# Performance work log

Hardware: AMD Instinct MI355X
Metric: run time of the kernel (lower is better)

The kernel has to match this reference:

```python
import jax, jax.numpy as jnp
import numpy as np

N = 65536      # total nodes (cells) in batch
E = 262144     # edges per edge type
T = 3          # edge types: row, col, diag
D = 128        # hidden_dim
HG = 4         # gat_heads
DHG = D // HG  # 32, GAT head dim
HH = 4         # hgt_heads
DHH = D // HH  # 32, HGT head dim
B = 32         # boards per batch
SLOPE = 0.2
EPS = 1e-6


def setup_inputs():
    ks = jax.random.split(jax.random.key(0), 32)
    def nrm(i, shape, s=0.05):
        return (jax.random.normal(ks[i], shape) * s).astype(jnp.float32)
    inp = {
        'x_cell': nrm(0, (N, D), 1.0),
        'z_h': nrm(1, (B, D), 1.0),
        'x_cell_embedded': nrm(2, (N, D), 1.0),
        'edge_index': jax.random.randint(ks[3], (T, 2, E), 0, N, dtype=jnp.int32),
        'batch_size': B,
        # GAT conv 1 (one GATConv per edge type, summed)
        'gat1_W': nrm(4, (T, D, D), 0.09),
        'gat1_asrc': nrm(5, (T, HG, DHG), 0.12),
        'gat1_adst': nrm(6, (T, HG, DHG), 0.12),
        'gat1_b': jnp.zeros((T, D), jnp.float32),
        # GAT conv 2
        'gat2_W': nrm(7, (T, D, D), 0.09),
        'gat2_asrc': nrm(8, (T, HG, DHG), 0.12),
        'gat2_adst': nrm(9, (T, HG, DHG), 0.12),
        'gat2_b': jnp.zeros((T, D), jnp.float32),
        # RMSNorms
        'norm1_s': jnp.ones((D,), jnp.float32),
        'norm2_s': jnp.ones((D,), jnp.float32),
        'norm3_s': jnp.ones((D,), jnp.float32),
        # HGT (single node type 'cell', T edge types)
        'hgt_Wk': nrm(10, (D, D), 0.09), 'hgt_bk': jnp.zeros((D,), jnp.float32),
        'hgt_Wq': nrm(11, (D, D), 0.09), 'hgt_bq': jnp.zeros((D,), jnp.float32),
        'hgt_Wv': nrm(12, (D, D), 0.09), 'hgt_bv': jnp.zeros((D,), jnp.float32),
        'hgt_arel': nrm(13, (T, HH, DHH, DHH), 0.15),
        'hgt_mrel': nrm(14, (T, HH, DHH, DHH), 0.15),
        'hgt_prel': jnp.ones((T, HH), jnp.float32),
        'hgt_Wo': nrm(15, (D, D), 0.09), 'hgt_bo': jnp.zeros((D,), jnp.float32),
        'hgt_skip': jnp.ones((), jnp.float32),
        # input injection
        'inj_W': nrm(16, (D, D), 0.09), 'inj_b': jnp.zeros((D,), jnp.float32),
        # FiLM
        'film_W1': nrm(17, (D, 2 * D), 0.09), 'film_b1': jnp.zeros((2 * D,), jnp.float32),
        'film_W2': nrm(18, (2 * D, 2 * D), 0.001), 'film_b2': jnp.zeros((2 * D,), jnp.float32),
    }
    return inp


def _rmsnorm(x, scale):
    return scale * x * jax.lax.rsqrt(jnp.mean(x * x, axis=-1, keepdims=True) + EPS)


def _res(x_old, x_new, scale):
    return jax.nn.leaky_relu(x_old + _rmsnorm(x_new, scale), SLOPE)


def _gat_sum(x, W, asrc, adst, b, src, dst):
    """HeteroConv(sum) over T GATConvs (concat heads, add_self_loops)."""
    loop = jnp.arange(N, dtype=src.dtype)
    def one(Wt, a_s, a_d, bt, s, t):
        s = jnp.concatenate([s, loop])   # self loops
        t = jnp.concatenate([t, loop])
        h = (x @ Wt).reshape(N, HG, DHG)             # [N,H,Dh]
        alpha_src = (h * a_s).sum(-1)                # [N,H]
        alpha_dst = (h * a_d).sum(-1)
        e = jax.nn.leaky_relu(alpha_src[s] + alpha_dst[t], SLOPE)  # [E+N,H]
        m = jax.ops.segment_max(e, t, num_segments=N)
        ex = jnp.exp(e - m[t])
        denom = jax.ops.segment_sum(ex, t, num_segments=N)
        alpha = ex / (denom[t] + 1e-16)
        out = jax.ops.segment_sum(alpha[:, :, None] * h[s], t, num_segments=N)
        return out.reshape(N, D) + bt
    return jax.vmap(one)(W, asrc, adst, b, src, dst).sum(0)


def _hgt(x, Wk, bk, Wq, bq, Wv, bv, a_rel, m_rel, p_rel, Wo, bo, skip, src, dst):
    k = (x @ Wk + bk).reshape(N, HH, DHH)
    q = (x @ Wq + bq).reshape(N, HH, DHH)
    v = (x @ Wv + bv).reshape(N, HH, DHH)
    # per-edge-type relation transforms at node level, then gather per edge
    k_t = jnp.einsum('nhd,thdf->tnhf', k, a_rel)    # [T,N,H,Dk]
    v_t = jnp.einsum('nhd,thdf->tnhf', v, m_rel)
    k_e = jax.vmap(lambda a, i: a[i])(k_t, src)     # [T,E,H,Dk]
    v_e = jax.vmap(lambda a, i: a[i])(v_t, src)
    score = (q[dst] * k_e).sum(-1) * p_rel[:, None, :] / np.sqrt(DHH)  # [T,E,H]
    score = score.reshape(T * E, HH)
    dst_f = dst.reshape(-1)
    m = jax.ops.segment_max(score, dst_f, num_segments=N)
    ex = jnp.exp(score - m[dst_f])
    denom = jax.ops.segment_sum(ex, dst_f, num_segments=N)
    alpha = ex / (denom[dst_f] + 1e-16)
    agg = jax.ops.segment_sum(alpha[:, :, None] * v_e.reshape(T * E, HH, DHH),
                              dst_f, num_segments=N)          # [N,H,Dk]
    out = jax.nn.gelu(agg.reshape(N, D), approximate=False) @ Wo + bo
    sig = jax.nn.sigmoid(skip)
    return sig * out + (1.0 - sig) * x


def _film(nodes, z_h, W1, b1, W2, b2, bsz):
    gb = jax.nn.gelu(z_h @ W1 + b1, approximate=False) @ W2 + b2  # [B,2D]
    gamma, beta = jnp.split(gb, 2, axis=-1)
    gamma = 0.1 * jnp.tanh(gamma)
    beta = 0.1 * jnp.tanh(beta)
    c = N // bsz
    out = (1.0 + gamma)[:, None, :] * nodes.reshape(bsz, c, D) + beta[:, None, :]
    return out.reshape(N, D)


def reference(x_cell, z_h, x_cell_embedded,
              gat1_W, gat1_asrc, gat1_adst, gat1_b,
              gat2_W, gat2_asrc, gat2_adst, gat2_b,
              norm1_s, norm2_s, norm3_s,
              hgt_Wk, hgt_bk, hgt_Wq, hgt_bq, hgt_Wv, hgt_bv,
              hgt_arel, hgt_mrel, hgt_prel, hgt_Wo, hgt_bo, hgt_skip,
              inj_W, inj_b, film_W1, film_b1, film_W2, film_b2,
              edge_index, batch_size):
    src = edge_index[:, 0]
    dst = edge_index[:, 1]
    x1 = _res(x_cell, _gat_sum(x_cell, gat1_W, gat1_asrc, gat1_adst, gat1_b, src, dst), norm1_s)
    x2 = _res(x1, _gat_sum(x1, gat2_W, gat2_asrc, gat2_adst, gat2_b, src, dst), norm2_s)
    x3 = _res(x2, _hgt(x2, hgt_Wk, hgt_bk, hgt_Wq, hgt_bq, hgt_Wv, hgt_bv,
                       hgt_arel, hgt_mrel, hgt_prel, hgt_Wo, hgt_bo, hgt_skip,
                       src, dst), norm3_s)
    x3 = x3 + x_cell_embedded @ inj_W + inj_b
    return _film(x3, z_h, film_W1, film_b1, film_W2, film_b2, batch_size)
```

## Files before the change

kernel.cpp:

```cpp
#include <hip/hip_runtime.h>

#define NN 65536
#define EE 262144
#define ND ((size_t)NN * 128)
#define TBW 132
#define WLP 136
#define NTOT (EE + NN)
#define CSRN (3*EE + 3*NN)

typedef unsigned short u16;
typedef short bf8_t __attribute__((ext_vector_type(8)));
typedef float f32x4 __attribute__((ext_vector_type(4)));

__device__ __forceinline__ float lrelu(float x){ return x > 0.f ? x : 0.2f*x; }
__device__ __forceinline__ float gelu_exact(float x){ return 0.5f*x*(1.f+erff(x*0.70710678118654752f)); }
__device__ __forceinline__ float fexp(float x){ return __expf(x); }
__device__ __forceinline__ u16 f2bf(float f){
    union { float f; unsigned u; } v; v.f = f;
    unsigned u = v.u;
    return (u16)((u + 0x7FFFu + ((u >> 16) & 1u)) >> 16);
}
__device__ __forceinline__ float bf2f(u16 b){
    union { unsigned u; float f; } v; v.u = ((unsigned)b) << 16; return v.f;
}
__device__ __forceinline__ float2 bf2x(unsigned p){
    union { unsigned u; float f; } a, b;
    a.u = (p & 0xFFFFu) << 16; b.u = p & 0xFFFF0000u;
    return make_float2(a.f, b.f);
}
__device__ __forceinline__ unsigned cvt2(float a, float b){
    unsigned r; asm("v_cvt_pk_bf16_f32 %0, %1, %2" : "=v"(r) : "v"(a), "v"(b)); return r;
}

__device__ __forceinline__ void load_af32(const float* __restrict__ X, int row, int lk, bf8_t* af){
    #pragma unroll
    for (int kk = 0; kk < 4; ++kk){
        const float* p = X + (size_t)row*128 + kk*32 + lk*8;
        float4 a = *(const float4*)p;
        float4 b = *(const float4*)(p+4);
        union { bf8_t v; unsigned u[4]; } r;
        r.u[0] = cvt2(a.x, a.y); r.u[1] = cvt2(a.z, a.w);
        r.u[2] = cvt2(b.x, b.y); r.u[3] = cvt2(b.z, b.w);
        af[kk] = r.v;
    }
}
__device__ __forceinline__ void load_af16(const u16* __restrict__ X, int row, int lk, bf8_t* af){
    #pragma unroll
    for (int kk = 0; kk < 4; ++kk)
        af[kk] = *(const bf8_t*)(X + (size_t)row*128 + kk*32 + lk*8);
}

__device__ __forceinline__ void stage_w(const u16* __restrict__ src, u16* __restrict__ wl, int tid){
    #pragma unroll
    for (int j = 0; j < 8; ++j){
        int o = (j*256 + tid)*8;
        bf8_t v = *(const bf8_t*)(src + o);
        *(bf8_t*)(wl + ((o>>7)*WLP + (o&127))) = v;
    }
}

__device__ __forceinline__ void mfma_l1_acc(const bf8_t* af, const u16* __restrict__ wl,
                                            int lr, int lk, f32x4* acc){
    #pragma unroll
    for (int kk = 0; kk < 4; ++kk){
        bf8_t B[8];
        #pragma unroll
        for (int nt = 0; nt < 8; ++nt)
            B[nt] = *(const bf8_t*)&wl[(nt*16+lr)*WLP + kk*32 + lk*8];
        #pragma unroll
        for (int nt = 0; nt < 8; ++nt)
            acc[nt] = __builtin_amdgcn_mfma_f32_16x16x32_bf16(af[kk], B[nt], acc[nt], 0, 0, 0);
    }
}
__device__ __forceinline__ void mfma_l1(const bf8_t* af, const u16* __restrict__ wl,
                                        int lr, int lk, f32x4* acc){
    #pragma unroll
    for (int i = 0; i < 8; ++i) acc[i] = (f32x4){0.f,0.f,0.f,0.f};
    mfma_l1_acc(af, wl, lr, lk, acc);
}
__device__ __forceinline__ void mfma_l2(const bf8_t* af0, const bf8_t* af1,
                                        const u16* __restrict__ wl,
                                        int lr, int lk, f32x4* acc0, f32x4* acc1){
    #pragma unroll
    for (int i = 0; i < 8; ++i){ acc0[i] = (f32x4){0.f,0.f,0.f,0.f}; acc1[i] = (f32x4){0.f,0.f,0.f,0.f}; }
    #pragma unroll
    for (int kk = 0; kk < 4; ++kk){
        bf8_t B[8];
        #pragma unroll
        for (int nt = 0; nt < 8; ++nt)
            B[nt] = *(const bf8_t*)&wl[(nt*16+lr)*WLP + kk*32 + lk*8];
        #pragma unroll
        for (int nt = 0; nt < 8; ++nt){
            acc0[nt] = __builtin_amdgcn_mfma_f32_16x16x32_bf16(af0[kk], B[nt], acc0[nt], 0, 0, 0);
            acc1[nt] = __builtin_amdgcn_mfma_f32_16x16x32_bf16(af1[kk], B[nt], acc1[nt], 0, 0, 0);
        }
    }
}
__device__ __forceinline__ void mfma_bd1_acc(const bf8_t* af, const u16* __restrict__ Bp,
                                             int lr, int lk, f32x4* acc){
    bf8_t B[8];
    #pragma unroll
    for (int nt = 0; nt < 8; ++nt)
        B[nt] = *(const bf8_t*)&Bp[nt*512 + lr*32 + lk*8];
    #pragma unroll
    for (int nt = 0; nt < 8; ++nt)
        acc[nt] = __builtin_amdgcn_mfma_f32_16x16x32_bf16(af[nt>>1], B[nt], acc[nt], 0, 0, 0);
}
__device__ __forceinline__ void mfma_bd2(const bf8_t* af0, const bf8_t* af1,
                                         const u16* __restrict__ Bp,
                                         int lr, int lk, f32x4* acc0, f32x4* acc1){
    bf8_t B[8];
    #pragma unroll
    for (int nt = 0; nt < 8; ++nt)
        B[nt] = *(const bf8_t*)&Bp[nt*512 + lr*32 + lk*8];
    #pragma unroll
    for (int nt = 0; nt < 8; ++nt){
        acc0[nt] = __builtin_amdgcn_mfma_f32_16x16x32_bf16(af0[nt>>1], B[nt], (f32x4){0.f,0.f,0.f,0.f}, 0, 0, 0);
        acc1[nt] = __builtin_amdgcn_mfma_f32_16x16x32_bf16(af1[nt>>1], B[nt], (f32x4){0.f,0.f,0.f,0.f}, 0, 0, 0);
    }
}

__device__ __forceinline__ void acc_to_tb(u16 (*tbw)[TBW], const f32x4* acc, int lr, int lk, const float* bias){
    asm volatile("s_waitcnt lgkmcnt(0)" ::: "memory");
    #pragma unroll
    for (int nt = 0; nt < 8; ++nt){
        int col = nt*16 + lr;
        float badd = bias ? bias[col] : 0.f;
        #pragma unroll
        for (int i = 0; i < 4; ++i) tbw[lk*4+i][col] = f2bf(acc[nt][i] + badd);
    }
    asm volatile("s_waitcnt lgkmcnt(0)" ::: "memory");
}
__device__ __forceinline__ void acc_to_tb_gelu(u16 (*tbw)[TBW], const f32x4* acc, int lr, int lk){
    asm volatile("s_waitcnt lgkmcnt(0)" ::: "memory");
    #pragma unroll
    for (int nt = 0; nt < 8; ++nt){
        int col = nt*16 + lr;
        #pragma unroll
        for (int i = 0; i < 4; ++i) tbw[lk*4+i][col] = f2bf(gelu_exact(acc[nt][i]));
    }
    asm volatile("s_waitcnt lgkmcnt(0)" ::: "memory");
}
__device__ __forceinline__ void tb_store(const u16 (*tbw)[TBW], u16* __restrict__ O, size_t rowstride, int rowbase, int lr, int lk){
    #pragma unroll
    for (int c = 0; c < 4; ++c){
        bf8_t v = *(const bf8_t*)&tbw[c*4+lk][lr*8];
        *(bf8_t*)(O + (size_t)(rowbase + c*4 + lk)*rowstride + lr*8) = v;
    }
}
__device__ __forceinline__ void tb_frags(const u16 (*tbw)[TBW], int lr, int lk, bf8_t* ha){
    #pragma unroll
    for (int kk = 0; kk < 4; ++kk) ha[kk] = *(const bf8_t*)&tbw[lr][kk*32 + lk*8];
}
__device__ __forceinline__ void tb_rows(const u16 (*tbw)[TBW], int lr, int lk, bf8_t* rw){
    #pragma unroll
    for (int c = 0; c < 4; ++c) rw[c] = *(const bf8_t*)&tbw[c*4+lk][lr*8];
}

__global__ __launch_bounds__(256) void wpack_k(
    const float* __restrict__ g1W, const float* __restrict__ g2W,
    const float* __restrict__ Wk, const float* __restrict__ Wq, const float* __restrict__ Wv,
    const float* __restrict__ Wo, const float* __restrict__ injW,
    const float* __restrict__ arel, const float* __restrict__ mrel,
    const float* __restrict__ g1as, const float* __restrict__ g1ad,
    const float* __restrict__ g2as, const float* __restrict__ g2ad,
    u16* __restrict__ wp, u16* __restrict__ wpa)
{
    int b = blockIdx.x, tid = threadIdx.x;
    if (b < 11) {
        const float* src;
        if (b < 3) src = g1W + b*16384;
        else if (b < 6) src = g2W + (b-3)*16384;
        else if (b == 6) src = Wk;
        else if (b == 7) src = Wq;
        else if (b == 8) src = Wv;
        else if (b == 9) src = Wo;
        else src = injW;
        u16* dst = wp + (size_t)b*16384;
        for (int idx = tid; idx < 16384; idx += 256) {
            int n = idx >> 7, k = idx & 127;
            dst[idx] = f2bf(src[k*128 + n]);
        }
    } else if (b < 17) {
        int rel2 = (b < 14);
        const float* src = rel2 ? (arel + (b-11)*4096) : (mrel + (b-14)*4096);
        u16* dst = wp + (size_t)11*16384 + (size_t)(b-11)*4096;
        for (int idx = tid; idx < 4096; idx += 256) {
            int nt = idx >> 9, rest = idx & 511;
            int lr = rest >> 5, kp = rest & 31;
            int h = nt >> 1, c = (nt & 1)*16 + lr;
            float v = rel2 ? src[h*1024 + c*32 + kp] : src[h*1024 + kp*32 + c];
            dst[idx] = f2bf(v);
        }
    } else {
        for (int idx = tid; idx < 6*2048; idx += 256) {
            int m = idx >> 11;
            int j = idx & 2047;
            int cg = j >> 7, k = j & 127;
            const float* as = (m < 3) ? g1as : g2as;
            const float* ad = (m < 3) ? g1ad : g2ad;
            int t = (m < 3) ? m : m - 3;
            float v = 0.f;
            if (cg < 4)      { if ((k>>5)==cg)   v = as[t*128 + cg*32 + (k&31)]; }
            else if (cg < 8) { int g = cg-4; if ((k>>5)==g) v = ad[t*128 + g*32 + (k&31)]; }
            wpa[idx] = f2bf(v);
        }
    }
}

template<int AF32>
__global__ __launch_bounds__(256, 3) void gat_gemm3_k(const float* __restrict__ Xf, const u16* __restrict__ Xb,
    const u16* __restrict__ wpg, const u16* __restrict__ wpa,
    u16* __restrict__ hb, float* __restrict__ alsb, float* __restrict__ aldb)
{
    __shared__ __align__(16) u16 wl[128*WLP];
    __shared__ __align__(16) u16 tb[4][16][TBW];
    const int tid = threadIdx.x, wave = tid>>6, lane = tid&63, lr = lane&15, lk = lane>>4;
    const int t = blockIdx.y;
    const int rw0 = blockIdx.x*128 + wave*32;
    bf8_t af0[4], af1[4];
    if (AF32){ load_af32(Xf, rw0 + lr, lk, af0); load_af32(Xf, rw0 + 16 + lr, lk, af1); }
    else     { load_af16(Xb, rw0 + lr, lk, af0); load_af16(Xb, rw0 + 16 + lr, lk, af1); }
    stage_w(wpg + t*16384, wl, tid);
    bf8_t Ba[4];
    #pragma unroll
    for (int kk = 0; kk < 4; ++kk)
        Ba[kk] = *(const bf8_t*)&wpa[t*2048 + lr*128 + kk*32 + lk*8];
    __syncthreads();
    f32x4 acc0[8], acc1[8];
    mfma_l2(af0, af1, wl, lr, lk, acc0, acc1);
    u16* h = hb + (size_t)t*ND;
    float* alst = alsb + (size_t)t*NN*4;
    float* aldt = aldb + (size_t)t*NN*4;
    {
        acc_to_tb(tb[wave], acc0, lr, lk, nullptr);
        tb_store(tb[wave], h, 128, rw0, lr, lk);
        bf8_t ha[4]; tb_frags(tb[wave], lr, lk, ha);
        f32x4 a2 = (f32x4){0.f,0.f,0.f,0.f};
        #pragma unroll
        for (int kk = 0; kk < 4; ++kk)
            a2 = __builtin_amdgcn_mfma_f32_16x16x32_bf16(ha[kk], Ba[kk], a2, 0, 0, 0);
        if (lr < 8){
            float* dp = (lr < 4) ? alst : aldt;
            int g = lr & 3;
            #pragma unroll
            for (int i = 0; i < 4; ++i) dp[(size_t)(rw0 + lk*4 + i)*4 + g] = a2[i];
        }
    }
    {
        acc_to_tb(tb[wave], acc1, lr, lk, nullptr);
        tb_store(tb[wave], h, 128, rw0 + 16, lr, lk);
        bf8_t ha[4]; tb_frags(tb[wave], lr, lk, ha);
        f32x4 a2 = (f32x4){0.f,0.f,0.f,0.f};
        #pragma unroll
        for (int kk = 0; kk < 4; ++kk)
            a2 = __builtin_amdgcn_mfma_f32_16x16x32_bf16(ha[kk], Ba[kk], a2, 0, 0, 0);
        if (lr < 8){
            float* dp = (lr < 4) ? alst : aldt;
            int g = lr & 3;
            #pragma unroll
            for (int i = 0; i < 4; ++i) dp[(size_t)(rw0 + 16 + lk*4 + i)*4 + g] = a2[i];
        }
    }
}

__global__ __launch_bounds__(256, 3) void hgt_proj_k(const u16* __restrict__ X,
    const u16* __restrict__ wpk, const u16* __restrict__ wpq, const u16* __restrict__ wpv,
    const u16* __restrict__ wpad,
    const float* __restrict__ bk, const float* __restrict__ bq, const float* __restrict__ bv,
    u16* __restrict__ kvb, u16* __restrict__ qtb)
{
    __shared__ __align__(16) u16 wl[128*WLP];
    __shared__ __align__(16) u16 tb[4][16][TBW];
    const int tid = threadIdx.x, wave = tid>>6, lane = tid&63, lr = lane&15, lk = lane>>4;
    const int task = blockIdx.y;
    const int rw0 = blockIdx.x*128 + wave*32;
    bf8_t af0[4], af1[4];
    load_af16(X, rw0 + lr, lk, af0);
    load_af16(X, rw0 + 16 + lr, lk, af1);
    f32x4 acc0[8], acc1[8];
    if (task == 0) {
        stage_w(wpk, wl, tid);
        __syncthreads();
        mfma_l2(af0, af1, wl, lr, lk, acc0, acc1);
        acc_to_tb(tb[wave], acc0, lr, lk, bk); tb_store(tb[wave], kvb, 256, rw0, lr, lk);
        acc_to_tb(tb[wave], acc1, lr, lk, bk); tb_store(tb[wave], kvb, 256, rw0 + 16, lr, lk);
    } else if (task == 1) {
        stage_w(wpv, wl, tid);
        __syncthreads();
        mfma_l2(af0, af1, wl, lr, lk, acc0, acc1);
        acc_to_tb(tb[wave], acc0, lr, lk, bv); tb_store(tb[wave], kvb + 128, 256, rw0, lr, lk);
        acc_to_tb(tb[wave], acc1, lr, lk, bv); tb_store(tb[wave], kvb + 128, 256, rw0 + 16, lr, lk);
    } else {
        const int t = task - 2;
        stage_w(wpq, wl, tid);
        __syncthreads();
        mfma_l2(af0, af1, wl, lr, lk, acc0, acc1);
        bf8_t ha0[4], ha1[4];
        acc_to_tb(tb[wave], acc0, lr, lk, bq); tb_frags(tb[wave], lr, lk, ha0);
        acc_to_tb(tb[wave], acc1, lr, lk, bq); tb_frags(tb[wave], lr, lk, ha1);
        mfma_bd2(ha0, ha1, wpad + t*4096, lr, lk, acc0, acc1);
        u16* o = qtb + (size_t)t*ND;
        acc_to_tb(tb[wave], acc0, lr, lk, nullptr); tb_store(tb[wave], o, 128, rw0, lr, lk);
        acc_to_tb(tb[wave], acc1, lr, lk, nullptr); tb_store(tb[wave], o, 128, rw0 + 16, lr, lk);
    }
}

__global__ __launch_bounds__(256) void hist_k(const int* __restrict__ ei, int* __restrict__ cnt){
    int gid = blockIdx.x*256 + threadIdx.x;
    int t = gid / EE, e = gid - t*EE;
    int d = ei[t*2*EE + EE + e];
    atomicAdd(&cnt[t*NN + d], 1);
}
__global__ __launch_bounds__(256) void scanA_k(const int* __restrict__ cnt, int* __restrict__ s0off, int* __restrict__ parts){
    __shared__ int sums[256];
    int b = blockIdx.x; int base = b * 1024;
    int tid = threadIdx.x;
    int v[4]; int tsum = 0;
    #pragma unroll
    for (int i = 0; i < 4; ++i){
        int n = base + tid*4 + i;
        v[i] = cnt[n] + cnt[NN+n] + cnt[2*NN+n] + 3;
        tsum += v[i];
    }
    sums[tid] = tsum; __syncthreads();
    for (int ofs = 1; ofs < 256; ofs <<= 1) {
        int a = (tid >= ofs) ? sums[tid-ofs] : 0;
        __syncthreads();
        sums[tid] += a;
        __syncthreads();
    }
    int run = sums[tid] - tsum;
    #pragma unroll
    for (int i = 0; i < 4; ++i){ s0off[base + tid*4 + i] = run; run += v[i]; }
    if (tid == 255) parts[b] = sums[255];
}
__global__ void scan2_k(int* parts){
    if (threadIdx.x == 0 && blockIdx.x == 0) {
        int run = 0;
        for (int i = 0; i < 64; ++i) { int v = parts[i]; parts[i] = run; run += v; }
    }
}
__global__ __launch_bounds__(256) void scanB_k(const int* __restrict__ cnt, int* __restrict__ s0off,
                                               int* __restrict__ s1off, int* __restrict__ s2off,
                                               const int* __restrict__ parts){
    int b = blockIdx.x; int base = b * 1024;
    int add = parts[b];
    #pragma unroll
    for (int i = 0; i < 4; ++i){
        int n = base + threadIdx.x*4 + i;
        int m = s0off[n] + add;
        int c0 = cnt[n], c1 = cnt[NN+n];
        s0off[n] = m;
        s1off[n] = m + c0 + 1;
        s2off[n] = m + c0 + c1 + 2;
    }
    if (b == 0 && threadIdx.x == 0) s0off[NN] = CSRN;
}
__global__ __launch_bounds__(256) void selffill_k(const int* __restrict__ s0off, const int* __restrict__ s1off,
                                                  const int* __restrict__ s2off, int* __restrict__ csrc){
    int gid = blockIdx.x*256 + threadIdx.x;
    int t = gid / NN, n = gid - t*NN;
    int pos = (t==0) ? s0off[n] : (t==1 ? s1off[n] : s2off[n]);
    csrc[pos] = n;
}
__global__ __launch_bounds__(256) void scatter_k(const int* __restrict__ ei,
    const int* __restrict__ s0off, const int* __restrict__ s1off, const int* __restrict__ s2off,
    int* __restrict__ cur, int* __restrict__ csrc, int* __restrict__ posmap){
    int gid = blockIdx.x*256 + threadIdx.x;
    int t = gid / EE, e = gid - t*EE;
    int s = ei[t*2*EE + e];
    int d = ei[t*2*EE + EE + e];
    int p = atomicAdd(&cur[t*NN + d], 1);
    int basep = (t==0) ? s0off[d] : (t==1 ? s1off[d] : s2off[d]);
    int pos = basep + 1 + p;
    csrc[pos] = s;
    posmap[t*EE + e] = pos;
}

__global__ __launch_bounds__(256) void alpha_k(const float* __restrict__ alsb, const float* __restrict__ aldb,
    const int* __restrict__ ei, const int* __restrict__ posmap,
    const int* __restrict__ s0off, const int* __restrict__ s1off, const int* __restrict__ s2off,
    float4* __restrict__ ab)
{
    int gid = blockIdx.x*256 + threadIdx.x;
    int t = gid / NTOT, r = gid - t*NTOT;
    int s, d, pos;
    if (r < EE) {
        s = ei[t*2*EE + r];
        d = ei[t*2*EE + EE + r];
        pos = posmap[t*EE + r];
    } else {
        int n = r - EE;
        s = n; d = n;
        pos = (t==0) ? s0off[n] : (t==1 ? s1off[n] : s2off[n]);
    }
    const float* As = alsb + ((size_t)t*NN + s)*4;
    const float* Ad = aldb + ((size_t)t*NN + d)*4;
    float4 o;
    o.x = fexp(lrelu(As[0] + Ad[0]));
    o.y = fexp(lrelu(As[1] + Ad[1]));
    o.z = fexp(lrelu(As[2] + Ad[2]));
    o.w = fexp(lrelu(As[3] + Ad[3]));
    ab[pos] = o;
}

template<int XF32>
__global__ __launch_bounds__(256) void gat_aggres_k(const u16* __restrict__ hb,
    const float* __restrict__ abf,
    const int* __restrict__ s0off, const int* __restrict__ s1off, const int* __restrict__ s2off,
    const int* __restrict__ csrc,
    const float* __restrict__ bias3, const float* __restrict__ xoldf, const u16* __restrict__ xoldb,
    const float* __restrict__ scale, u16* __restrict__ outb)
{
    int gid = blockIdx.x*256 + threadIdx.x;
    int node = gid >> 6, lane = gid & 63;
    int eh = lane >> 5, hh = (lane >> 3) & 3, cp = lane & 7;
    int ch = hh*32 + cp*4;
    int segb[4] = { s0off[node], s1off[node], s2off[node], s0off[node+1] };
    float a[4] = {0.f, 0.f, 0.f, 0.f};
    #pragma unroll
    for (int t = 0; t < 3; ++t) {
        const u16* h = hb + (size_t)t*ND;
        int beg = segb[t], end = segb[t+1];
        float ds = 0.f, s0 = 0.f, s1 = 0.f, s2 = 0.f, s3 = 0.f;
        for (int pos = beg; pos < end; pos += 4) {
            int p0 = pos + eh, p1 = pos + 2 + eh;
            int v0 = (p0 < end), v1 = (p1 < end);
            int q0 = v0 ? p0 : beg, q1 = v1 ? p1 : beg;
            int sA = csrc[q0], sB = csrc[q1];
            float alA = abf[(size_t)q0*4 + hh];
            float alB = abf[(size_t)q1*4 + hh];
            uint2 hA = *(const uint2*)&h[(size_t)sA*128 + ch];
            uint2 hB = *(const uint2*)&h[(size_t)sB*128 + ch];
            alA = v0 ? alA : 0.f;
            alB = v1 ? alB : 0.f;
            float2 wA0 = bf2x(hA.x), wA1 = bf2x(hA.y);
            float2 wB0 = bf2x(hB.x), wB1 = bf2x(hB.y);
            ds += alA + alB;
            s0 += alA*wA0.x + alB*wB0.x;
            s1 += alA*wA0.y + alB*wB0.y;
            s2 += alA*wA1.x + alB*wB1.x;
            s3 += alA*wA1.y + alB*wB1.y;
        }
        ds += __shfl_xor(ds, 32);
        s0 += __shfl_xor(s0, 32);
        s1 += __shfl_xor(s1, 32);
        s2 += __shfl_xor(s2, 32);
        s3 += __shfl_xor(s3, 32);
        float inv = 1.f/(ds + 1e-16f);
        a[0] += s0*inv; a[1] += s1*inv; a[2] += s2*inv; a[3] += s3*inv;
    }
    float4 b0 = *(const float4*)&bias3[ch];
    float4 b1 = *(const float4*)&bias3[128 + ch];
    float4 b2 = *(const float4*)&bias3[256 + ch];
    a[0] += b0.x + b1.x + b2.x;
    a[1] += b0.y + b1.y + b2.y;
    a[2] += b0.z + b1.z + b2.z;
    a[3] += b0.w + b1.w + b2.w;
    float ssum = a[0]*a[0] + a[1]*a[1] + a[2]*a[2] + a[3]*a[3];
    ssum += __shfl_xor(ssum, 1); ssum += __shfl_xor(ssum, 2);
    ssum += __shfl_xor(ssum, 4); ssum += __shfl_xor(ssum, 8);
    ssum += __shfl_xor(ssum, 16);
    float r = rsqrtf(ssum*(1.f/128.f) + 1e-6f);
    float4 sc = *(const float4*)&scale[ch];
    size_t off = (size_t)node*128 + ch;
    float x0, x1v, x2v, x3;
    if (XF32) {
        float4 xo = *(const float4*)&xoldf[off];
        x0 = xo.x; x1v = xo.y; x2v = xo.z; x3 = xo.w;
    } else {
        uint2 xo = *(const uint2*)&xoldb[off];
        float2 p0 = bf2x(xo.x), p1 = bf2x(xo.y);
        x0 = p0.x; x1v = p0.y; x2v = p1.x; x3 = p1.y;
    }
    float y0 = lrelu(x0  + sc.x*a[0]*r);
    float y1 = lrelu(x1v + sc.y*a[1]*r);
    float y2 = lrelu(x2v + sc.z*a[2]*r);
    float y3 = lrelu(x3  + sc.w*a[3]*r);
    uint2 o2; o2.x = cvt2(y0, y1); o2.y = cvt2(y2, y3);
    *(uint2*)&outb[off] = o2;
}

__global__ __launch_bounds__(256) void hgt_agg_k(const u16* __restrict__ kvb,
    const u16* __restrict__ qtb, const float* __restrict__ prel,
    const int* __restrict__ s0off, const int* __restrict__ s1off, const int* __restrict__ s2off,
    const int* __restrict__ csrc, u16* __restrict__ pb)
{
    int gid = blockIdx.x*256 + threadIdx.x;
    int node = gid >> 6, lane = gid & 63;
    int eh = lane >> 5, hh = (lane >> 3) & 3, cp = lane & 7;
    int ch = hh*32 + cp*4;
    const float S = 0.17677669529663689f;
    int segb[4] = { s0off[node], s1off[node], s2off[node], s0off[node+1] };
    float dsum = 0.f;
    float ac[3][4];
    #pragma unroll
    for (int t = 0; t < 3; ++t){ ac[t][0]=0.f; ac[t][1]=0.f; ac[t][2]=0.f; ac[t][3]=0.f; }
    #pragma unroll
    for (int t = 0; t < 3; ++t) {
        float ph = prel[t*4 + hh] * S;
        uint2 qw = *(const uint2*)&qtb[(size_t)t*ND + (size_t)node*128 + ch];
        float2 q0 = bf2x(qw.x), q1 = bf2x(qw.y);
        int self = segb[t];
        int beg = self + 1, end = segb[t+1];
        for (int pos = beg; pos < end; pos += 4) {
            int p0 = pos + eh, p1 = pos + 2 + eh;
            int v0 = (p0 < end), v1 = (p1 < end);
            int qp0 = v0 ? p0 : self, qp1 = v1 ? p1 : self;
            int sA = csrc[qp0], sB = csrc[qp1];
            size_t rA = (size_t)sA*256 + ch, rB = (size_t)sB*256 + ch;
            uint2 kA = *(const uint2*)&kvb[rA], kB = *(const uint2*)&kvb[rB];
            uint2 vA = *(const uint2*)&kvb[rA + 128], vB = *(const uint2*)&kvb[rB + 128];
            float2 kA0 = bf2x(kA.x), kA1 = bf2x(kA.y);
            float2 kB0 = bf2x(kB.x), kB1 = bf2x(kB.y);
            float scA = kA0.x*q0.x + kA0.y*q0.y + kA1.x*q1.x + kA1.y*q1.y;
            float scB = kB0.x*q0.x + kB0.y*q0.y + kB1.x*q1.x + kB1.y*q1.y;
            scA += __shfl_xor(scA, 1); scB += __shfl_xor(scB, 1);
            scA += __shfl_xor(scA, 2); scB += __shfl_xor(scB, 2);
            scA += __shfl_xor(scA, 4); scB += __shfl_xor(scB, 4);
            float eA = v0 ? fexp(scA*ph) : 0.f;
            float eB = v1 ? fexp(scB*ph) : 0.f;
            float2 vA0 = bf2x(vA.x), vA1 = bf2x(vA.y);
            float2 vB0 = bf2x(vB.x), vB1 = bf2x(vB.y);
            dsum += eA + eB;
            ac[t][0] += eA*vA0.x + eB*vB0.x;
            ac[t][1] += eA*vA0.y + eB*vB0.y;
            ac[t][2] += eA*vA1.x + eB*vB1.x;
            ac[t][3] += eA*vA1.y + eB*vB1.y;
        }
    }
    dsum += __shfl_xor(dsum, 32);
    #pragma unroll
    for (int t = 0; t < 3; ++t){
        ac[t][0] += __shfl_xor(ac[t][0], 32);
        ac[t][1] += __shfl_xor(ac[t][1], 32);
        ac[t][2] += __shfl_xor(ac[t][2], 32);
        ac[t][3] += __shfl_xor(ac[t][3], 32);
    }
    float inv = 1.f/(dsum + 1e-16f);
    size_t o = (size_t)node*128 + ch;
    #pragma unroll
    for (int t = 0; t < 3; ++t){
        uint2 o2;
        o2.x = cvt2(ac[t][0]*inv, ac[t][1]*inv);
        o2.y = cvt2(ac[t][2]*inv, ac[t][3]*inv);
        *(uint2*)&pb[(size_t)t*ND + o] = o2;
    }
}

__global__ __launch_bounds__(256, 3) void final_k(const u16* __restrict__ pb,
    const u16* __restrict__ wpmd, const u16* __restrict__ wpo, const float* __restrict__ bo,
    const u16* __restrict__ x2b, const float* __restrict__ skipp, const float* __restrict__ scale,
    const float* __restrict__ xemb, const u16* __restrict__ wpinj, const float* __restrict__ injb,
    const float* __restrict__ gbuf, const int* __restrict__ bszp,
    float* __restrict__ out)
{
    __shared__ __align__(16) u16 wl[128*WLP];
    __shared__ __align__(16) u16 tb[4][16][TBW];
    const int tid = threadIdx.x, wave = tid>>6, lane = tid&63, lr = lane&15, lk = lane>>4;
    const int rw = blockIdx.x*64 + wave*16;
    stage_w(wpo, wl, tid);
    bf8_t e0[4];
    load_af32(xemb, rw + lr, lk, e0);
    f32x4 acc[8];
    #pragma unroll
    for (int i = 0; i < 8; ++i) acc[i] = (f32x4){0.f,0.f,0.f,0.f};
    #pragma unroll
    for (int t = 0; t < 3; ++t){
        bf8_t a0[4]; load_af16(pb + (size_t)t*ND, rw + lr, lk, a0);
        mfma_bd1_acc(a0, wpmd + t*4096, lr, lk, acc);
    }
    bf8_t ga[4];
    acc_to_tb_gelu(tb[wave], acc, lr, lk);
    tb_frags(tb[wave], lr, lk, ga);
    __syncthreads();
    mfma_l1(ga, wl, lr, lk, acc);
    bf8_t hw[4];
    acc_to_tb(tb[wave], acc, lr, lk, bo);
    tb_rows(tb[wave], lr, lk, hw);
    __syncthreads();
    stage_w(wpinj, wl, tid);
    __syncthreads();
    mfma_l1(e0, wl, lr, lk, acc);
    bf8_t in[4];
    acc_to_tb(tb[wave], acc, lr, lk, injb);
    tb_rows(tb[wave], lr, lk, in);
    const float sig = 1.f/(1.f + expf(-skipp[0]));
    const int cpb = NN / *bszp;
    float4 sca = *(const float4*)&scale[lr*8];
    float4 scb = *(const float4*)&scale[lr*8 + 4];
    #pragma unroll
    for (int c = 0; c < 4; ++c){
        int row = rw + c*4 + lk;
        bf8_t x8 = *(const bf8_t*)(x2b + (size_t)row*128 + lr*8);
        float x[8], v[8];
        float ssl = 0.f;
        #pragma unroll
        for (int j = 0; j < 8; ++j){
            x[j] = bf2f((u16)x8[j]);
            float h = bf2f((u16)hw[c][j]);
            v[j] = sig*h + (1.f - sig)*x[j];
            ssl += v[j]*v[j];
        }
        ssl += __shfl_xor(ssl, 1); ssl += __shfl_xor(ssl, 2);
        ssl += __shfl_xor(ssl, 4); ssl += __shfl_xor(ssl, 8);
        float rq = rsqrtf(ssl*(1.f/128.f) + 1e-6f);
        const float* gr = gbuf + (row / cpb)*256;
        float4 g0 = *(const float4*)&gr[lr*8];
        float4 g1 = *(const float4*)&gr[lr*8 + 4];
        float4 b0 = *(const float4*)&gr[128 + lr*8];
        float4 b1 = *(const float4*)&gr[128 + lr*8 + 4];
        float4 oA, oB;
        #pragma unroll
        for (int j = 0; j < 8; ++j){
            float scj = (j < 4) ? ((const float*)&sca)[j] : ((const float*)&scb)[j-4];
            float y = lrelu(x[j] + scj*v[j]*rq);
            float hf = y + bf2f((u16)in[c][j]);
            float gj = (j < 4) ? ((const float*)&g0)[j] : ((const float*)&g1)[j-4];
            float bj = (j < 4) ? ((const float*)&b0)[j] : ((const float*)&b1)[j-4];
            float ov = (1.f + gj)*hf + bj;
            if (j < 4) ((float*)&oA)[j] = ov; else ((float*)&oB)[j-4] = ov;
        }
        *(float4*)(out + (size_t)row*128 + lr*8)     = oA;
        *(float4*)(out + (size_t)row*128 + lr*8 + 4) = oB;
    }
}

__global__ __launch_bounds__(256) void film_k(const float* __restrict__ z,
    const float* __restrict__ W1, const float* __restrict__ b1,
    const float* __restrict__ W2, const float* __restrict__ b2,
    float* __restrict__ gb)
{
    __shared__ float zr[128];
    __shared__ float g1[256];
    int r = blockIdx.x, tid = threadIdx.x;
    if (tid < 128) zr[tid] = z[r*128 + tid];
    __syncthreads();
    float s = b1[tid];
    for (int k = 0; k < 128; ++k) s += zr[k]*W1[k*256 + tid];
    g1[tid] = gelu_exact(s);
    __syncthreads();
    float s2 = b2[tid];
    for (int k = 0; k < 256; ++k) s2 += g1[k]*W2[k*256 + tid];
    gb[r*256 + tid] = 0.1f*tanhf(s2);
}

extern "C" void kernel_launch(void* const* d_in, const int* in_sizes, int n_in,
                              void* d_out, int out_size, void* d_ws, size_t ws_size,
                              hipStream_t stream)
{
    const float* x_cell = (const float*)d_in[0];
    const float* z_h    = (const float*)d_in[1];
    const float* x_emb  = (const float*)d_in[2];
    const int*   eidx   = (const int*)d_in[3];
    const int*   bszp   = (const int*)d_in[4];
    const float* g1W  = (const float*)d_in[5];
    const float* g1as = (const float*)d_in[6];
    const float* g1ad = (const float*)d_in[7];
    const float* g1b  = (const float*)d_in[8];
    const float* g2W  = (const float*)d_in[9];
    const float* g2as = (const float*)d_in[10];
    const float* g2ad = (const float*)d_in[11];
    const float* g2b  = (const float*)d_in[12];
    const float* n1s  = (const float*)d_in[13];
    const float* n2s  = (const float*)d_in[14];
    const float* n3s  = (const float*)d_in[15];
    const float* Wk   = (const float*)d_in[16];
    const float* bk   = (const float*)d_in[17];
    const float* Wq   = (const float*)d_in[18];
    const float* bq   = (const float*)d_in[19];
    const float* Wv   = (const float*)d_in[20];
    const float* bv   = (const float*)d_in[21];
    const float* arel = (const float*)d_in[22];
    const float* mrel = (const float*)d_in[23];
    const float* prel = (const float*)d_in[24];
    const float* Wo   = (const float*)d_in[25];
    const float* bo   = (const float*)d_in[26];
    const float* skipp= (const float*)d_in[27];
    const float* injW = (const float*)d_in[28];
    const float* injb = (const float*)d_in[29];
    const float* fW1  = (const float*)d_in[30];
    const float* fb1  = (const float*)d_in[31];
    const float* fW2  = (const float*)d_in[32];
    const float* fb2  = (const float*)d_in[33];

    u16* wp   = (u16*)d_ws;
    u16* wpa  = wp + (size_t)17*16384;
    float4* ab = (float4*)(wpa + 6*2048);
    u16* x1b  = (u16*)(ab + CSRN);
    u16* x2b  = x1b + ND;
    u16* kvb  = x2b + ND;
    u16* pb   = kvb + 2*ND;
    u16* hb   = pb + 3*ND;
    float* alsb = (float*)(hb + 3*ND);
    float* aldb = alsb + (size_t)3*NN*4;
    float* gbuf = aldb + (size_t)3*NN*4;
    int* s0off  = (int*)(gbuf + 32*256);
    int* s1off  = s0off + (NN+1);
    int* s2off  = s1off + NN;
    int* csrc   = s2off + NN;
    int* posmap = csrc + CSRN;
    int* tmpc   = posmap + 3*EE;
    int* cur    = tmpc + 3*NN;
    int* parts  = cur + 3*NN;

    u16* qtb = hb;
    float* outp = (float*)d_out;

    const u16* wpg1 = wp;
    const u16* wpg2 = wp + (size_t)3*16384;
    const u16* wpk  = wp + (size_t)6*16384;
    const u16* wpq  = wp + (size_t)7*16384;
    const u16* wpv  = wp + (size_t)8*16384;
    const u16* wpo  = wp + (size_t)9*16384;
    const u16* wpinj= wp + (size_t)10*16384;
    const u16* wpad = wp + (size_t)11*16384;
    const u16* wpmd = wpad + (size_t)3*4096;

    wpack_k<<<18, 256, 0, stream>>>(g1W, g2W, Wk, Wq, Wv, Wo, injW, arel, mrel,
                                    g1as, g1ad, g2as, g2ad, wp, wpa);

    hipMemsetAsync(tmpc, 0, 3*NN*sizeof(int), stream);
    hist_k<<<3*EE/256, 256, 0, stream>>>(eidx, tmpc);
    scanA_k<<<64, 256, 0, stream>>>(tmpc, s0off, parts);
    scan2_k<<<1, 64, 0, stream>>>(parts);
    scanB_k<<<64, 256, 0, stream>>>(tmpc, s0off, s1off, s2off, parts);
    selffill_k<<<3*NN/256, 256, 0, stream>>>(s0off, s1off, s2off, csrc);
    hipMemsetAsync(cur, 0, 3*NN*sizeof(int), stream);
    scatter_k<<<3*EE/256, 256, 0, stream>>>(eidx, s0off, s1off, s2off, cur, csrc, posmap);

    int B = in_sizes[1] / 128;
    film_k<<<B, 256, 0, stream>>>(z_h, fW1, fb1, fW2, fb2, gbuf);

    gat_gemm3_k<1><<<dim3(512,3), 256, 0, stream>>>(x_cell, nullptr, wpg1, wpa, hb, alsb, aldb);
    alpha_k<<<3*NTOT/256, 256, 0, stream>>>(alsb, aldb, eidx, posmap, s0off, s1off, s2off, ab);
    gat_aggres_k<1><<<16384, 256, 0, stream>>>(hb, (const float*)ab, s0off, s1off, s2off, csrc,
                                               g1b, x_cell, nullptr, n1s, x1b);

    gat_gemm3_k<0><<<dim3(512,3), 256, 0, stream>>>(nullptr, x1b, wpg2, wpa + 3*2048, hb, alsb, aldb);
    alpha_k<<<3*NTOT/256, 256, 0, stream>>>(alsb, aldb, eidx, posmap, s0off, s1off, s2off, ab);
    gat_aggres_k<0><<<16384, 256, 0, stream>>>(hb, (const float*)ab, s0off, s1off, s2off, csrc,
                                               g2b, nullptr, x1b, n2s, x2b);

    hgt_proj_k<<<dim3(512,5), 256, 0, stream>>>(x2b, wpk, wpq, wpv, wpad,
                                                bk, bq, bv, kvb, qtb);
    hgt_agg_k<<<16384, 256, 0, stream>>>(kvb, qtb, prel, s0off, s1off, s2off, csrc, pb);

    final_k<<<1024, 256, 0, stream>>>(pb, wpmd, wpo, bo, x2b, skipp, n3s,
                                      x_emb, wpinj, injb, gbuf, bszp, outp);
}
```

Measured before the change: 562.9 us.

## Store HGT key/value in FP8 and pre-cast input features to bf16

The HGT key and value projections are now written as FP8 (e4m3) instead of bf16, and the HGT aggregation decodes them with packed FP8-to-f32 conversions. This halves the bytes gathered per edge in the irregular neighbour loop. A new cast kernel converts x_cell to bf16 once, so both GAT layers share one bf16 input path. The FP8 storage costs numerical accuracy in attention scores and values, and the residual for layer one now uses the bf16-rounded input, while the cast kernel adds an extra launch and full pass over x_cell.

New measurement: 540.9 us. 1.04x faster.

```diff
diff --git a/kernel.cpp b/kernel.cpp
--- a/kernel.cpp
+++ b/kernel.cpp
@@ -9,8 +9,10 @@
 #define CSRN (3*EE + 3*NN)
 
 typedef unsigned short u16;
+typedef unsigned char u8;
 typedef short bf8_t __attribute__((ext_vector_type(8)));
 typedef float f32x4 __attribute__((ext_vector_type(4)));
+typedef float f32x2 __attribute__((ext_vector_type(2)));
 
 __device__ __forceinline__ float lrelu(float x){ return x > 0.f ? x : 0.2f*x; }
 __device__ __forceinline__ float gelu_exact(float x){ return 0.5f*x*(1.f+erff(x*0.70710678118654752f)); }
@@ -30,6 +32,11 @@
 }
 __device__ __forceinline__ unsigned cvt2(float a, float b){
     unsigned r; asm("v_cvt_pk_bf16_f32 %0, %1, %2" : "=v"(r) : "v"(a), "v"(b)); return r;
+}
+__device__ __forceinline__ unsigned enc_fp8x4(float a, float b, float c, float d){
+    int r = __builtin_amdgcn_cvt_pk_fp8_f32(a, b, 0, false);
+    r = __builtin_amdgcn_cvt_pk_fp8_f32(c, d, r, true);
+    return (unsigned)r;
 }
 
 __device__ __forceinline__ void load_af32(const float* __restrict__ X, int row, int lk, bf8_t* af){
@@ -148,6 +155,19 @@
         *(bf8_t*)(O + (size_t)(rowbase + c*4 + lk)*rowstride + lr*8) = v;
     }
 }
+__device__ __forceinline__ void tb_store_fp8(const u16 (*tbw)[TBW], u8* __restrict__ O, size_t rowstride, int rowbase, int lr, int lk){
+    #pragma unroll
+    for (int c = 0; c < 4; ++c){
+        bf8_t v = *(const bf8_t*)&tbw[c*4+lk][lr*8];
+        float f[8];
+        #pragma unroll
+        for (int j = 0; j < 8; ++j) f[j] = bf2f((u16)v[j]);
+        uint2 o2;
+        o2.x = enc_fp8x4(f[0], f[1], f[2], f[3]);
+        o2.y = enc_fp8x4(f[4], f[5], f[6], f[7]);
+        *(uint2*)(O + (size_t)(rowbase + c*4 + lk)*rowstride + lr*8) = o2;
+    }
+}
 __device__ __forceinline__ void tb_frags(const u16 (*tbw)[TBW], int lr, int lk, bf8_t* ha){
     #pragma unroll
     for (int kk = 0; kk < 4; ++kk) ha[kk] = *(const bf8_t*)&tbw[lr][kk*32 + lk*8];
@@ -155,6 +175,17 @@
 __device__ __forceinline__ void tb_rows(const u16 (*tbw)[TBW], int lr, int lk, bf8_t* rw){
     #pragma unroll
     for (int c = 0; c < 4; ++c) rw[c] = *(const bf8_t*)&tbw[c*4+lk][lr*8];
+}
+
+__global__ __launch_bounds__(256) void xcast_k(const float* __restrict__ X, u16* __restrict__ O){
+    size_t gid = (size_t)blockIdx.x*256 + threadIdx.x;
+    const float* p = X + gid*8;
+    float4 a = *(const float4*)p;
+    float4 b = *(const float4*)(p+4);
+    union { bf8_t v; unsigned u[4]; } r;
+    r.u[0] = cvt2(a.x, a.y); r.u[1] = cvt2(a.z, a.w);
+    r.u[2] = cvt2(b.x, b.y); r.u[3] = cvt2(b.z, b.w);
+    *(bf8_t*)(O + gid*8) = r.v;
 }
 
 __global__ __launch_bounds__(256) void wpack_k(
@@ -208,8 +239,7 @@
     }
 }
 
-template<int AF32>
-__global__ __launch_bounds__(256, 3) void gat_gemm3_k(const float* __restrict__ Xf, const u16* __restrict__ Xb,
+__global__ __launch_bounds__(256, 3) void gat_gemm3_k(const u16* __restrict__ Xb,
     const u16* __restrict__ wpg, const u16* __restrict__ wpa,
     u16* __restrict__ hb, float* __restrict__ alsb, float* __restrict__ aldb)
 {
@@ -219,8 +249,8 @@
     const int t = blockIdx.y;
     const int rw0 = blockIdx.x*128 + wave*32;
     bf8_t af0[4], af1[4];
-    if (AF32){ load_af32(Xf, rw0 + lr, lk, af0); load_af32(Xf, rw0 + 16 + lr, lk, af1); }
-    else     { load_af16(Xb, rw0 + lr, lk, af0); load_af16(Xb, rw0 + 16 + lr, lk, af1); }
+    load_af16(Xb, rw0 + lr, lk, af0);
+    load_af16(Xb, rw0 + 16 + lr, lk, af1);
     stage_w(wpg + t*16384, wl, tid);
     bf8_t Ba[4];
     #pragma unroll
@@ -268,7 +298,7 @@
     const u16* __restrict__ wpk, const u16* __restrict__ wpq, const u16* __restrict__ wpv,
     const u16* __restrict__ wpad,
     const float* __restrict__ bk, const float* __restrict__ bq, const float* __restrict__ bv,
-    u16* __restrict__ kvb, u16* __restrict__ qtb)
+    u8* __restrict__ kvb, u16* __restrict__ qtb)
 {
     __shared__ __align__(16) u16 wl[128*WLP];
     __shared__ __align__(16) u16 tb[4][16][TBW];
@@ -283,14 +313,14 @@
         stage_w(wpk, wl, tid);
         __syncthreads();
         mfma_l2(af0, af1, wl, lr, lk, acc0, acc1);
-        acc_to_tb(tb[wave], acc0, lr, lk, bk); tb_store(tb[wave], kvb, 256, rw0, lr, lk);
-        acc_to_tb(tb[wave], acc1, lr, lk, bk); tb_store(tb[wave], kvb, 256, rw0 + 16, lr, lk);
+        acc_to_tb(tb[wave], acc0, lr, lk, bk); tb_store_fp8(tb[wave], kvb, 256, rw0, lr, lk);
+        acc_to_tb(tb[wave], acc1, lr, lk, bk); tb_store_fp8(tb[wave], kvb, 256, rw0 + 16, lr, lk);
     } else if (task == 1) {
         stage_w(wpv, wl, tid);
         __syncthreads();
         mfma_l2(af0, af1, wl, lr, lk, acc0, acc1);
-        acc_to_tb(tb[wave], acc0, lr, lk, bv); tb_store(tb[wave], kvb + 128, 256, rw0, lr, lk);
-        acc_to_tb(tb[wave], acc1, lr, lk, bv); tb_store(tb[wave], kvb + 128, 256, rw0 + 16, lr, lk);
+        acc_to_tb(tb[wave], acc0, lr, lk, bv); tb_store_fp8(tb[wave], kvb + 128, 256, rw0, lr, lk);
+        acc_to_tb(tb[wave], acc1, lr, lk, bv); tb_store_fp8(tb[wave], kvb + 128, 256, rw0 + 16, lr, lk);
     } else {
         const int t = task - 2;
         stage_w(wpq, wl, tid);
@@ -405,12 +435,11 @@
     ab[pos] = o;
 }
 
-template<int XF32>
 __global__ __launch_bounds__(256) void gat_aggres_k(const u16* __restrict__ hb,
     const float* __restrict__ abf,
     const int* __restrict__ s0off, const int* __restrict__ s1off, const int* __restrict__ s2off,
     const int* __restrict__ csrc,
-    const float* __restrict__ bias3, const float* __restrict__ xoldf, const u16* __restrict__ xoldb,
+    const float* __restrict__ bias3, const u16* __restrict__ xoldb,
     const float* __restrict__ scale, u16* __restrict__ outb)
 {
     int gid = blockIdx.x*256 + threadIdx.x;
@@ -465,24 +494,17 @@
     float r = rsqrtf(ssum*(1.f/128.f) + 1e-6f);
     float4 sc = *(const float4*)&scale[ch];
     size_t off = (size_t)node*128 + ch;
-    float x0, x1v, x2v, x3;
-    if (XF32) {
-        float4 xo = *(const float4*)&xoldf[off];
-        x0 = xo.x; x1v = xo.y; x2v = xo.z; x3 = xo.w;
-    } else {
-        uint2 xo = *(const uint2*)&xoldb[off];
-        float2 p0 = bf2x(xo.x), p1 = bf2x(xo.y);
-        x0 = p0.x; x1v = p0.y; x2v = p1.x; x3 = p1.y;
-    }
-    float y0 = lrelu(x0  + sc.x*a[0]*r);
-    float y1 = lrelu(x1v + sc.y*a[1]*r);
-    float y2 = lrelu(x2v + sc.z*a[2]*r);
-    float y3 = lrelu(x3  + sc.w*a[3]*r);
+    uint2 xo = *(const uint2*)&xoldb[off];
+    float2 p0 = bf2x(xo.x), p1 = bf2x(xo.y);
+    float y0 = lrelu(p0.x + sc.x*a[0]*r);
+    float y1 = lrelu(p0.y + sc.y*a[1]*r);
+    float y2 = lrelu(p1.x + sc.z*a[2]*r);
+    float y3 = lrelu(p1.y + sc.w*a[3]*r);
     uint2 o2; o2.x = cvt2(y0, y1); o2.y = cvt2(y2, y3);
     *(uint2*)&outb[off] = o2;
 }
 
-__global__ __launch_bounds__(256) void hgt_agg_k(const u16* __restrict__ kvb,
+__global__ __launch_bounds__(256) void hgt_agg_k(const u8* __restrict__ kvb,
     const u16* __restrict__ qtb, const float* __restrict__ prel,
     const int* __restrict__ s0off, const int* __restrict__ s1off, const int* __restrict__ s2off,
     const int* __restrict__ csrc, u16* __restrict__ pb)
@@ -510,24 +532,28 @@
             int qp0 = v0 ? p0 : self, qp1 = v1 ? p1 : self;
             int sA = csrc[qp0], sB = csrc[qp1];
             size_t rA = (size_t)sA*256 + ch, rB = (size_t)sB*256 + ch;
-            uint2 kA = *(const uint2*)&kvb[rA], kB = *(const uint2*)&kvb[rB];
-            uint2 vA = *(const uint2*)&kvb[rA + 128], vB = *(const uint2*)&kvb[rB + 128];
-            float2 kA0 = bf2x(kA.x), kA1 = bf2x(kA.y);
-            float2 kB0 = bf2x(kB.x), kB1 = bf2x(kB.y);
-            float scA = kA0.x*q0.x + kA0.y*q0.y + kA1.x*q1.x + kA1.y*q1.y;
-            float scB = kB0.x*q0.x + kB0.y*q0.y + kB1.x*q1.x + kB1.y*q1.y;
+            unsigned kA = *(const unsigned*)&kvb[rA], kB = *(const unsigned*)&kvb[rB];
+            unsigned vA = *(const unsigned*)&kvb[rA + 128], vB = *(const unsigned*)&kvb[rB + 128];
+            f32x2 kA0 = __builtin_amdgcn_cvt_pk_f32_fp8((int)kA, false);
+            f32x2 kA1 = __builtin_amdgcn_cvt_pk_f32_fp8((int)kA, true);
+            f32x2 kB0 = __builtin_amdgcn_cvt_pk_f32_fp8((int)kB, false);
+            f32x2 kB1 = __builtin_amdgcn_cvt_pk_f32_fp8((int)kB, true);
+            float scA = kA0[0]*q0.x + kA0[1]*q0.y + kA1[0]*q1.x + kA1[1]*q1.y;
+            float scB = kB0[0]*q0.x + kB0[1]*q0.y + kB1[0]*q1.x + kB1[1]*q1.y;
             scA += __shfl_xor(scA, 1); scB += __shfl_xor(scB, 1);
             scA += __shfl_xor(scA, 2); scB += __shfl_xor(scB, 2);
             scA += __shfl_xor(scA, 4); scB += __shfl_xor(scB, 4);
             float eA = v0 ? fexp(scA*ph) : 0.f;
             float eB = v1 ? fexp(scB*ph) : 0.f;
-            float2 vA0 = bf2x(vA.x), vA1 = bf2x(vA.y);
-            float2 vB0 = bf2x(vB.x), vB1 = bf2x(vB.y);
+            f32x2 vA0 = __builtin_amdgcn_cvt_pk_f32_fp8((int)vA, false);
+            f32x2 vA1 = __builtin_amdgcn_cvt_pk_f32_fp8((int)vA, true);
+            f32x2 vB0 = __builtin_amdgcn_cvt_pk_f32_fp8((int)vB, false);
+            f32x2 vB1 = __builtin_amdgcn_cvt_pk_f32_fp8((int)vB, true);
             dsum += eA + eB;
-            ac[t][0] += eA*vA0.x + eB*vB0.x;
-            ac[t][1] += eA*vA0.y + eB*vB0.y;
-            ac[t][2] += eA*vA1.x + eB*vB1.x;
-            ac[t][3] += eA*vA1.y + eB*vB1.y;
+            ac[t][0] += eA*vA0[0] + eB*vB0[0];
+            ac[t][1] += eA*vA0[1] + eB*vB0[1];
+            ac[t][2] += eA*vA1[0] + eB*vB1[0];
+            ac[t][3] += eA*vA1[1] + eB*vB1[1];
         }
     }
     dsum += __shfl_xor(dsum, 32);
@@ -688,10 +714,11 @@
     u16* wp   = (u16*)d_ws;
     u16* wpa  = wp + (size_t)17*16384;
     float4* ab = (float4*)(wpa + 6*2048);
-    u16* x1b  = (u16*)(ab + CSRN);
+    u16* x0b  = (u16*)(ab + CSRN);
+    u16* x1b  = x0b + ND;
     u16* x2b  = x1b + ND;
-    u16* kvb  = x2b + ND;
-    u16* pb   = kvb + 2*ND;
+    u8*  kvb  = (u8*)(x2b + ND);
+    u16* pb   = (u16*)(kvb + (size_t)NN*256);
     u16* hb   = pb + 3*ND;
     float* alsb = (float*)(hb + 3*ND);
     float* aldb = alsb + (size_t)3*NN*4;
@@ -720,6 +747,7 @@
 
     wpack_k<<<18, 256, 0, stream>>>(g1W, g2W, Wk, Wq, Wv, Wo, injW, arel, mrel,
                                     g1as, g1ad, g2as, g2ad, wp, wpa);
+    xcast_k<<<(int)(ND/2048), 256, 0, stream>>>(x_cell, x0b);
 
     hipMemsetAsync(tmpc, 0, 3*NN*sizeof(int), stream);
     hist_k<<<3*EE/256, 256, 0, stream>>>(eidx, tmpc);
@@ -733,15 +761,15 @@
     int B = in_sizes[1] / 128;
     film_k<<<B, 256, 0, stream>>>(z_h, fW1, fb1, fW2, fb2, gbuf);
 
-    gat_gemm3_k<1><<<dim3(512,3), 256, 0, stream>>>(x_cell, nullptr, wpg1, wpa, hb, alsb, aldb);
+    gat_gemm3_k<<<dim3(512,3), 256, 0, stream>>>(x0b, wpg1, wpa, hb, alsb, aldb);
     alpha_k<<<3*NTOT/256, 256, 0, stream>>>(alsb, aldb, eidx, posmap, s0off, s1off, s2off, ab);
-    gat_aggres_k<1><<<16384, 256, 0, stream>>>(hb, (const float*)ab, s0off, s1off, s2off, csrc,
-                                               g1b, x_cell, nullptr, n1s, x1b);
-
-    gat_gemm3_k<0><<<dim3(512,3), 256, 0, stream>>>(nullptr, x1b, wpg2, wpa + 3*2048, hb, alsb, aldb);
+    gat_aggres_k<<<16384, 256, 0, stream>>>(hb, (const float*)ab, s0off, s1off, s2off, csrc,
+                                            g1b, x0b, n1s, x1b);
+
+    gat_gemm3_k<<<dim3(512,3), 256, 0, stream>>>(x1b, wpg2, wpa + 3*2048, hb, alsb, aldb);
     alpha_k<<<3*NTOT/256, 256, 0, stream>>>(alsb, aldb, eidx, posmap, s0off, s1off, s2off, ab);
-    gat_aggres_k<0><<<16384, 256, 0, stream>>>(hb, (const float*)ab, s0off, s1off, s2off, csrc,
-                                               g2b, nullptr, x1b, n2s, x2b);
+    gat_aggres_k<<<16384, 256, 0, stream>>>(hb, (const float*)ab, s0off, s1off, s2off, csrc,
+                                            g2b, x1b, n2s, x2b);
 
     hgt_proj_k<<<dim3(512,5), 256, 0, stream>>>(x2b, wpk, wpq, wpv, wpad,
                                                 bk, bq, bv, kvb, qtb);
```
